# Optimization experiments

Hardware: AMD Instinct MI355X
Metric: run time of the kernel (lower is better)

Reference implementation:

```python
import jax, jax.numpy as jnp
import numpy as np

N_NODES = 50000
N_EDGES = 800000
N_GRAPHS = 512
IN_C, HID, OUT_C = 128, 256, 16


def _mlp(h, w1, b1, w2, b2):
    # PyG-style 2-layer MLP: Linear -> ReLU -> Linear (plain last layer)
    return jax.nn.relu(h @ w1 + b1) @ w2 + b2


def setup_inputs() -> dict:
    key = jax.random.key(0)
    ks = jax.random.split(key, 16)
    x = jax.random.normal(ks[0], (N_NODES, IN_C), dtype=jnp.float32)
    edge_index = jax.random.randint(ks[1], (2, N_EDGES), 0, N_NODES, dtype=jnp.int64)
    batch = jnp.sort(jax.random.randint(ks[2], (N_NODES,), 0, N_GRAPHS, dtype=jnp.int64))

    def lin(k, fan_in, fan_out):
        s = 1.0 / np.sqrt(fan_in)
        return jax.random.uniform(k, (fan_in, fan_out), jnp.float32, -s, s)

    inp = {"x": x, "edge_index": edge_index, "batch": batch}
    dims = [(IN_C, HID), (HID, HID), (HID, HID)]
    ki = 3
    for li, (din, dh) in enumerate(dims):
        inp[f"c{li}_w1"] = lin(ks[ki], din, dh); ki += 1
        inp[f"c{li}_b1"] = jnp.zeros((dh,), jnp.float32)
        inp[f"c{li}_w2"] = lin(ks[ki], dh, dh); ki += 1
        inp[f"c{li}_b2"] = jnp.zeros((dh,), jnp.float32)
    inp["out_w1"] = lin(ks[ki], HID, HID); ki += 1
    inp["out_b1"] = jnp.zeros((HID,), jnp.float32)
    inp["out_w2"] = lin(ks[ki], HID, OUT_C); ki += 1
    inp["out_b2"] = jnp.zeros((OUT_C,), jnp.float32)
    return inp


def reference(x, edge_index, batch,
              c0_w1, c0_b1, c0_w2, c0_b2,
              c1_w1, c1_b1, c1_w2, c1_b2,
              c2_w1, c2_b1, c2_w2, c2_b2,
              out_w1, out_b1, out_w2, out_b2):
    src, dst = edge_index[0], edge_index[1]
    params = [(c0_w1, c0_b1, c0_w2, c0_b2),
              (c1_w1, c1_b1, c1_w2, c1_b2),
              (c2_w1, c2_b1, c2_w2, c2_b2)]
    h = x
    for (w1, b1, w2, b2) in params:
        # GINConv with eps=0: MLP(x + sum_{j in N(i)} x_j)
        agg = jax.ops.segment_sum(h[src], dst, num_segments=N_NODES)
        h = _mlp(h + agg, w1, b1, w2, b2)
        h = jax.nn.relu(h)
        # dropout: identity (eval mode)
    # global mean pool over graphs
    sums = jax.ops.segment_sum(h, batch, num_segments=N_GRAPHS)
    counts = jax.ops.segment_sum(jnp.ones((N_NODES,), h.dtype), batch, num_segments=N_GRAPHS)
    pooled = sums / jnp.maximum(counts, 1.0)[:, None]
    return _mlp(pooled, out_w1, out_b1, out_w2, out_b2)
```

## Files before the change

kernel.cpp:

```cpp
#include <hip/hip_runtime.h>

#define N_NODES 50000
#define N_EDGES 800000
#define N_GRAPHS 512
#define IN_C 128
#define HID 256
#define OUT_C 16

typedef __attribute__((ext_vector_type(8))) short short8;
typedef __attribute__((ext_vector_type(4))) float f32x4;

__device__ __forceinline__ float bf2f(unsigned short u) {
    return __uint_as_float(((unsigned int)u) << 16);
}
__device__ __forceinline__ unsigned short f2bf(float f) {
    unsigned int u = __float_as_uint(f);
    u += 0x7fff + ((u >> 16) & 1);
    return (unsigned short)(u >> 16);
}

#define PLANE_ELEMS ((long)N_NODES * 32)

struct PrepArgs {
    const float* x;
    const float* w[6];
    ushort* xbf;
    ushort* wt[6];
    int* deg;
    float* sums;
};

__global__ __launch_bounds__(256) void prep_kernel(PrepArgs a) {
    const int X4    = N_NODES * IN_C / 4;
    const int TW    = IN_C * HID;
    const int TH    = HID * HID;
    const int TBASE = X4;
    const int TEND  = TBASE + TW + 5 * TH;
    const int D4    = N_NODES / 4;
    const int DBASE = TEND;
    const int SBASE = DBASE + D4;
    const int S4    = N_GRAPHS * HID / 4;
    const long total = (long)SBASE + S4;

    long stride = (long)gridDim.x * blockDim.x;
    for (long i = (long)blockIdx.x * blockDim.x + threadIdx.x; i < total; i += stride) {
        if (i < X4) {
            float4 v = ((const float4*)a.x)[i];
            ushort4 o;
            o.x = f2bf(v.x); o.y = f2bf(v.y); o.z = f2bf(v.z); o.w = f2bf(v.w);
            long e = i * 4;
            int node = (int)(e >> 7);
            int col  = (int)(e & 127);
            long off = (long)(col >> 5) * PLANE_ELEMS + (long)node * 32 + (col & 31);
            *(ushort4*)(a.xbf + off) = o;
        } else if (i < TEND) {
            long r = i - TBASE;
            int wi, shift;
            long off;
            if (r < TW) { wi = 0; shift = 7; off = r; }
            else { r -= TW; wi = 1 + (int)(r / TH); shift = 8; off = r % TH; }
            int n = (int)(off >> shift);
            int k = (int)(off - ((long)n << shift));
            a.wt[wi][off] = f2bf(a.w[wi][(long)k * HID + n]);
        } else if (i < SBASE) {
            ((int4*)a.deg)[i - DBASE] = make_int4(0, 0, 0, 0);
        } else {
            ((float4*)a.sums)[i - SBASE] = make_float4(0.f, 0.f, 0.f, 0.f);
        }
    }
}

__global__ void deg_kernel(const int* __restrict__ dst, int* __restrict__ deg) {
    int e = blockIdx.x * blockDim.x + threadIdx.x;
    if (e < N_EDGES) atomicAdd(&deg[dst[e]], 1);
}

__global__ __launch_bounds__(256) void scan_block(const int* __restrict__ deg,
                                                  int* __restrict__ partial,
                                                  int* __restrict__ blockSums) {
    __shared__ int s[256];
    int t = threadIdx.x;
    int i = blockIdx.x * 256 + t;
    int v = (i < N_NODES) ? deg[i] : 0;
    s[t] = v;
    __syncthreads();
    #pragma unroll
    for (int off = 1; off < 256; off <<= 1) {
        int add = (t >= off) ? s[t - off] : 0;
        __syncthreads();
        s[t] += add;
        __syncthreads();
    }
    if (i < N_NODES) partial[i] = s[t] - v;
    if (t == 255) blockSums[blockIdx.x] = s[255];
}

__global__ __launch_bounds__(256) void add_offsets_fused(
    const int* __restrict__ partial, const int* __restrict__ blockSums,
    int* __restrict__ rowptr, int* __restrict__ cursor, int nb) {
    __shared__ int s[256];
    __shared__ int myOff;
    int t = threadIdx.x;
    int v = (t < nb) ? blockSums[t] : 0;
    s[t] = v;
    __syncthreads();
    #pragma unroll
    for (int off = 1; off < 256; off <<= 1) {
        int add = (t >= off) ? s[t - off] : 0;
        __syncthreads();
        s[t] += add;
        __syncthreads();
    }
    if (t == blockIdx.x) myOff = s[t] - v;
    __syncthreads();
    int i = blockIdx.x * 256 + t;
    if (i < N_NODES) {
        int r = partial[i] + myOff;
        rowptr[i] = r;
        cursor[i] = r;
    }
    if (i == 0) rowptr[N_NODES] = N_EDGES;
}

__global__ void bucket_edges(const int* __restrict__ src, const int* __restrict__ dst,
                             int* __restrict__ cursor, int* __restrict__ srcSorted) {
    int e = blockIdx.x * blockDim.x + threadIdx.x;
    if (e >= N_EDGES) return;
    int p = atomicAdd(&cursor[dst[e]], 1);
    srcSorted[p] = src[e];
}

template <int C>
__global__ __launch_bounds__(256) void gin_aggregate_planar(
    const ushort* __restrict__ hp,
    const int* __restrict__ rowptr,
    const int* __restrict__ srcIdx,
    ushort* __restrict__ out)
{
    constexpr int NC  = C / 32;
    constexpr int PER = 8 / NC;

    int b  = blockIdx.x;
    int x8 = b & 7;
    int chunk   = x8 / PER;
    int nodeblk = (b >> 3) * PER + (x8 & (PER - 1));

    int lane = threadIdx.x & 63;
    int wave = threadIdx.x >> 6;
    int grp  = lane >> 2;
    int l    = lane & 3;
    int node = nodeblk * 64 + wave * 16 + grp;
    if (node >= N_NODES) return;

    const ushort* plane = hp + (long)chunk * PLANE_ELEMS + l * 8;

    float acc[8];
    {
        short8 sv = *(const short8*)(plane + (long)node * 32);
        #pragma unroll
        for (int v = 0; v < 8; ++v) acc[v] = bf2f((unsigned short)sv[v]);
    }

    int beg = rowptr[node], end = rowptr[node + 1];
    int k = beg;
    for (; k + 4 <= end; k += 4) {
        int si[4];
        #pragma unroll
        for (int u = 0; u < 4; ++u) si[u] = srcIdx[k + u];
        short8 r[4];
        #pragma unroll
        for (int u = 0; u < 4; ++u) r[u] = *(const short8*)(plane + (long)si[u] * 32);
        #pragma unroll
        for (int u = 0; u < 4; ++u)
            #pragma unroll
            for (int v = 0; v < 8; ++v) acc[v] += bf2f((unsigned short)r[u][v]);
    }
    for (; k < end; ++k) {
        short8 r = *(const short8*)(plane + (long)srcIdx[k] * 32);
        #pragma unroll
        for (int v = 0; v < 8; ++v) acc[v] += bf2f((unsigned short)r[v]);
    }

    short8 o;
    #pragma unroll
    for (int v = 0; v < 8; ++v) o[v] = (short)f2bf(acc[v]);
    *(short8*)(out + (long)node * C + chunk * 32 + l * 8) = o;
}

template <int K1, bool FUSE_POOL>
__global__ __launch_bounds__(256, 4) void gin_mlp(
    const ushort* __restrict__ A,
    const ushort* __restrict__ w1t,
    const float* __restrict__ b1,
    const ushort* __restrict__ w2t,
    const float* __restrict__ b2,
    ushort* __restrict__ out,
    const int* __restrict__ batch,
    float* __restrict__ sums,
    int M)
{
    __shared__ short Ls[2048 * 8];

    constexpr int NCH1 = K1 / 8;
    constexpr int NSLOT1 = 64 * NCH1;

    int t = threadIdx.x;
    int lane = t & 63;
    int wv = t >> 6;
    int quad = lane >> 4;
    int l15 = lane & 15;
    int swz = l15 & 7;
    int row0 = blockIdx.x * 64;
    int col0 = wv * 64;

    #pragma unroll
    for (int c = 0; c < NSLOT1; c += 256) {
        int s = c + t;
        int row = s / NCH1;
        int kcs = s & (NCH1 - 1);
        int kc = kcs ^ (row & 7);
        int grow = row0 + row;
        if (grow >= M) grow = M - 1;
        short8 v = *(const short8*)(A + (long)grow * K1 + kc * 8);
        *(short8*)&Ls[s * 8] = v;
    }
    __syncthreads();

    const f32x4 zero = {0.f, 0.f, 0.f, 0.f};
    f32x4 acc[4][4];

    #pragma unroll
    for (int i = 0; i < 4; ++i)
        #pragma unroll
        for (int j = 0; j < 4; ++j) acc[i][j] = zero;

    long brow[4];
    #pragma unroll
    for (int j = 0; j < 4; ++j)
        brow[j] = (long)(col0 + j * 16 + l15) * K1;

    #pragma unroll
    for (int s = 0; s < K1 / 32; ++s) {
        short8 a[4], b[4];
        #pragma unroll
        for (int i = 0; i < 4; ++i) {
            int row = i * 16 + l15;
            int slot = row * NCH1 + ((s * 4 + quad) ^ swz);
            a[i] = *(const short8*)&Ls[slot * 8];
        }
        #pragma unroll
        for (int j = 0; j < 4; ++j)
            b[j] = *(const short8*)(w1t + brow[j] + s * 32 + quad * 8);
        #pragma unroll
        for (int i = 0; i < 4; ++i)
            #pragma unroll
            for (int j = 0; j < 4; ++j)
                acc[i][j] = __builtin_amdgcn_mfma_f32_16x16x32_bf16(a[i], b[j], acc[i][j], 0, 0, 0);
    }
    __syncthreads();

    {
        float bv[4];
        #pragma unroll
        for (int j = 0; j < 4; ++j) bv[j] = b1[col0 + j * 16 + l15];
        #pragma unroll
        for (int i = 0; i < 4; ++i)
            #pragma unroll
            for (int j = 0; j < 4; ++j) {
                int col = col0 + j * 16 + l15;
                int kc2 = col >> 3, sub = col & 7;
                #pragma unroll
                for (int r = 0; r < 4; ++r) {
                    int row = i * 16 + quad * 4 + r;
                    int slot = row * 32 + (kc2 ^ (row & 7));
                    float o = fmaxf(acc[i][j][r] + bv[j], 0.f);
                    Ls[slot * 8 + sub] = (short)f2bf(o);
                }
            }
    }
    __syncthreads();

    #pragma unroll
    for (int i = 0; i < 4; ++i)
        #pragma unroll
        for (int j = 0; j < 4; ++j) acc[i][j] = zero;

    long brow2[4];
    #pragma unroll
    for (int j = 0; j < 4; ++j)
        brow2[j] = (long)(col0 + j * 16 + l15) * 256;

    #pragma unroll
    for (int s = 0; s < 8; ++s) {
        short8 a[4], b[4];
        #pragma unroll
        for (int i = 0; i < 4; ++i) {
            int row = i * 16 + l15;
            int slot = row * 32 + ((s * 4 + quad) ^ swz);
            a[i] = *(const short8*)&Ls[slot * 8];
        }
        #pragma unroll
        for (int j = 0; j < 4; ++j)
            b[j] = *(const short8*)(w2t + brow2[j] + s * 32 + quad * 8);
        #pragma unroll
        for (int i = 0; i < 4; ++i)
            #pragma unroll
            for (int j = 0; j < 4; ++j)
                acc[i][j] = __builtin_amdgcn_mfma_f32_16x16x32_bf16(a[i], b[j], acc[i][j], 0, 0, 0);
    }

    float bv[4];
    #pragma unroll
    for (int j = 0; j < 4; ++j) bv[j] = b2[col0 + j * 16 + l15];

    if constexpr (!FUSE_POOL) {
        #pragma unroll
        for (int i = 0; i < 4; ++i)
            #pragma unroll
            for (int r = 0; r < 4; ++r) {
                int row = row0 + i * 16 + quad * 4 + r;
                if (row >= M) continue;
                #pragma unroll
                for (int j = 0; j < 4; ++j) {
                    int col = col0 + j * 16 + l15;
                    float o = fmaxf(acc[i][j][r] + bv[j], 0.f);
                    out[(long)(col >> 5) * PLANE_ELEMS + (long)row * 32 + (col & 31)] = f2bf(o);
                }
            }
    } else {
        float pacc[4];
        #pragma unroll
        for (int j = 0; j < 4; ++j) pacc[j] = 0.f;
        int cur = -1;
        #pragma unroll
        for (int i = 0; i < 4; ++i) {
            #pragma unroll
            for (int r = 0; r < 4; ++r) {
                int row = row0 + i * 16 + quad * 4 + r;
                if (row >= M) continue;
                int g = batch[row];
                if (g != cur) {
                    if (cur >= 0) {
                        #pragma unroll
                        for (int j = 0; j < 4; ++j)
                            atomicAdd(&sums[(long)cur * 256 + col0 + j * 16 + l15], pacc[j]);
                    }
                    cur = g;
                    #pragma unroll
                    for (int j = 0; j < 4; ++j) pacc[j] = 0.f;
                }
                #pragma unroll
                for (int j = 0; j < 4; ++j)
                    pacc[j] += fmaxf(acc[i][j][r] + bv[j], 0.f);
            }
        }
        if (cur >= 0) {
            #pragma unroll
            for (int j = 0; j < 4; ++j)
                atomicAdd(&sums[(long)cur * 256 + col0 + j * 16 + l15], pacc[j]);
        }
    }
}

__global__ __launch_bounds__(256) void final_mlp_kernel(
    const float* __restrict__ sums, const int* __restrict__ batch,
    const float* __restrict__ w1, const float* __restrict__ b1,
    const float* __restrict__ w2, const float* __restrict__ b2,
    float* __restrict__ out) {
    __shared__ float row[HID];
    __shared__ float hid[HID];
    __shared__ int cntS;
    int g = blockIdx.x;
    int t = threadIdx.x;
    if (t == 0) {
        int lo = 0, hi = N_NODES;
        while (lo < hi) { int m = (lo + hi) >> 1; if (batch[m] < g) lo = m + 1; else hi = m; }
        int lo2 = lo, hi2 = N_NODES;
        while (lo2 < hi2) { int m = (lo2 + hi2) >> 1; if (batch[m] < g + 1) lo2 = m + 1; else hi2 = m; }
        cntS = lo2 - lo;
    }
    __syncthreads();
    float cnt = fmaxf((float)cntS, 1.0f);
    row[t] = sums[(long)g * HID + t] / cnt;
    __syncthreads();
    float acc = b1[t];
    for (int k = 0; k < HID; ++k) acc += row[k] * w1[k * HID + t];
    hid[t] = fmaxf(acc, 0.f);
    __syncthreads();
    if (t < OUT_C) {
        float o = b2[t];
        for (int k = 0; k < HID; ++k) o += hid[k] * w2[k * OUT_C + t];
        out[(long)g * OUT_C + t] = o;
    }
}

extern "C" void kernel_launch(void* const* d_in, const int* in_sizes, int n_in,
                              void* d_out, int out_size, void* d_ws, size_t ws_size,
                              hipStream_t stream) {
    const float* x     = (const float*)d_in[0];
    const int*   ei    = (const int*)d_in[1];
    const int*   batch = (const int*)d_in[2];
    const int*   src   = ei;
    const int*   dst   = ei + N_EDGES;

    const float* c_w1[3] = { (const float*)d_in[3],  (const float*)d_in[7],  (const float*)d_in[11] };
    const float* c_b1[3] = { (const float*)d_in[4],  (const float*)d_in[8],  (const float*)d_in[12] };
    const float* c_w2[3] = { (const float*)d_in[5],  (const float*)d_in[9],  (const float*)d_in[13] };
    const float* c_b2[3] = { (const float*)d_in[6],  (const float*)d_in[10], (const float*)d_in[14] };
    const float* out_w1 = (const float*)d_in[15];
    const float* out_b1 = (const float*)d_in[16];
    const float* out_w2 = (const float*)d_in[17];
    const float* out_b2 = (const float*)d_in[18];

    char* p = (char*)d_ws;
    auto alloc = [&](size_t bytes) {
        char* r = p;
        p += (bytes + 15) & ~(size_t)15;
        return r;
    };
    ushort* xbf  = (ushort*)alloc((size_t)N_NODES * IN_C * 2);
    ushort* bufA = (ushort*)alloc((size_t)N_NODES * HID * 2);
    ushort* bufB = (ushort*)alloc((size_t)N_NODES * HID * 2);
    ushort* wt[6];
    wt[0] = (ushort*)alloc((size_t)IN_C * HID * 2);
    for (int i = 1; i < 6; ++i) wt[i] = (ushort*)alloc((size_t)HID * HID * 2);
    float* sums   = (float*)alloc((size_t)N_GRAPHS * HID * 4);
    int* deg       = (int*)alloc((size_t)N_NODES * 4);
    int* rowptr    = (int*)alloc((size_t)(N_NODES + 1) * 4);
    int* blockSums = (int*)alloc(256 * 4);
    int* cursor    = (int*)alloc((size_t)N_NODES * 4);
    int* srcSorted = (int*)alloc((size_t)N_EDGES * 4);

    const int nb = (N_NODES + 255) / 256;

    {
        PrepArgs a;
        a.x = x;
        a.w[0] = c_w1[0]; a.w[1] = c_w2[0];
        a.w[2] = c_w1[1]; a.w[3] = c_w2[1];
        a.w[4] = c_w1[2]; a.w[5] = c_w2[2];
        a.xbf = xbf;
        for (int i = 0; i < 6; ++i) a.wt[i] = wt[i];
        a.deg = deg;
        a.sums = sums;
        prep_kernel<<<2048, 256, 0, stream>>>(a);
    }

    deg_kernel<<<(N_EDGES + 255) / 256, 256, 0, stream>>>(dst, deg);
    scan_block<<<nb, 256, 0, stream>>>(deg, rowptr, blockSums);
    add_offsets_fused<<<nb, 256, 0, stream>>>(rowptr, blockSums, rowptr, cursor, nb);
    bucket_edges<<<(N_EDGES + 255) / 256, 256, 0, stream>>>(src, dst, cursor, srcSorted);

    const int nodeBlks = (N_NODES + 63) / 64;
    const int aggX128  = nodeBlks * (IN_C / 32);
    const int aggX256  = nodeBlks * (HID / 32);
    const int mlpGrid  = (N_NODES + 63) / 64;

    gin_aggregate_planar<IN_C><<<aggX128, 256, 0, stream>>>(xbf, rowptr, srcSorted, bufB);
    gin_mlp<IN_C, false><<<mlpGrid, 256, 0, stream>>>(bufB, wt[0], c_b1[0], wt[1], c_b2[0],
                                                      bufA, batch, sums, N_NODES);

    gin_aggregate_planar<HID><<<aggX256, 256, 0, stream>>>(bufA, rowptr, srcSorted, bufB);
    gin_mlp<HID, false><<<mlpGrid, 256, 0, stream>>>(bufB, wt[2], c_b1[1], wt[3], c_b2[1],
                                                     bufA, batch, sums, N_NODES);

    gin_aggregate_planar<HID><<<aggX256, 256, 0, stream>>>(bufA, rowptr, srcSorted, bufB);
    gin_mlp<HID, true><<<mlpGrid, 256, 0, stream>>>(bufB, wt[4], c_b1[2], wt[5], c_b2[2],
                                                    bufA, batch, sums, N_NODES);

    final_mlp_kernel<<<N_GRAPHS, 256, 0, stream>>>(sums, batch, out_w1, out_b1,
                                                   out_w2, out_b2, (float*)d_out);
}
```

Measured before the change: 464.3 us.

## Use 8 waves per MLP block and hold weight fragments in registers

The fused GIN MLP kernel now launches 512 threads (8 waves), and each wave computes 32 output columns instead of 64. Each wave preloads all of its layer-1 weight fragments into registers before the A tile is staged. It then loads its layer-2 weights during the epilogue, instead of fetching B fragments inside the MFMA loop. This is meant to raise wave-level parallelism and hide global weight-load latency behind the LDS staging and MFMA work. The cost is more register pressure from the 16 short8 fragments, and each A fragment read from LDS now feeds only two MFMAs, which lowers arithmetic intensity per LDS read.

```diff
diff --git a/kernel.cpp b/kernel.cpp
--- a/kernel.cpp
+++ b/kernel.cpp
@@ -188,7 +188,7 @@
 }
 
 template <int K1, bool FUSE_POOL>
-__global__ __launch_bounds__(256, 4) void gin_mlp(
+__global__ __launch_bounds__(512, 4) void gin_mlp(
     const ushort* __restrict__ A,
     const ushort* __restrict__ w1t,
     const float* __restrict__ b1,
@@ -203,6 +203,7 @@
 
     constexpr int NCH1 = K1 / 8;
     constexpr int NSLOT1 = 64 * NCH1;
+    constexpr int NS1 = K1 / 32;
 
     int t = threadIdx.x;
     int lane = t & 63;
@@ -211,10 +212,21 @@
     int l15 = lane & 15;
     int swz = l15 & 7;
     int row0 = blockIdx.x * 64;
-    int col0 = wv * 64;
-
-    #pragma unroll
-    for (int c = 0; c < NSLOT1; c += 256) {
+    int col0 = wv * 32;
+
+    short8 bw[16];
+    #pragma unroll
+    for (int s = 0; s < NS1; ++s)
+        #pragma unroll
+        for (int j = 0; j < 2; ++j)
+            bw[s * 2 + j] = *(const short8*)(w1t + (long)(col0 + j * 16 + l15) * K1 + s * 32 + quad * 8);
+
+    float bv[2];
+    #pragma unroll
+    for (int j = 0; j < 2; ++j) bv[j] = b1[col0 + j * 16 + l15];
+
+    #pragma unroll
+    for (int c = 0; c < NSLOT1; c += 512) {
         int s = c + t;
         int row = s / NCH1;
         int kcs = s & (NCH1 - 1);
@@ -227,91 +239,68 @@
     __syncthreads();
 
     const f32x4 zero = {0.f, 0.f, 0.f, 0.f};
-    f32x4 acc[4][4];
-
+    f32x4 acc[4][2];
     #pragma unroll
     for (int i = 0; i < 4; ++i)
         #pragma unroll
-        for (int j = 0; j < 4; ++j) acc[i][j] = zero;
-
-    long brow[4];
-    #pragma unroll
-    for (int j = 0; j < 4; ++j)
-        brow[j] = (long)(col0 + j * 16 + l15) * K1;
-
-    #pragma unroll
-    for (int s = 0; s < K1 / 32; ++s) {
-        short8 a[4], b[4];
+        for (int j = 0; j < 2; ++j) acc[i][j] = zero;
+
+    #pragma unroll
+    for (int s = 0; s < NS1; ++s) {
         #pragma unroll
         for (int i = 0; i < 4; ++i) {
             int row = i * 16 + l15;
             int slot = row * NCH1 + ((s * 4 + quad) ^ swz);
-            a[i] = *(const short8*)&Ls[slot * 8];
-        }
-        #pragma unroll
-        for (int j = 0; j < 4; ++j)
-            b[j] = *(const short8*)(w1t + brow[j] + s * 32 + quad * 8);
-        #pragma unroll
-        for (int i = 0; i < 4; ++i)
+            short8 a = *(const short8*)&Ls[slot * 8];
+            acc[i][0] = __builtin_amdgcn_mfma_f32_16x16x32_bf16(a, bw[s * 2 + 0], acc[i][0], 0, 0, 0);
+            acc[i][1] = __builtin_amdgcn_mfma_f32_16x16x32_bf16(a, bw[s * 2 + 1], acc[i][1], 0, 0, 0);
+        }
+    }
+
+    #pragma unroll
+    for (int s = 0; s < 8; ++s)
+        #pragma unroll
+        for (int j = 0; j < 2; ++j)
+            bw[s * 2 + j] = *(const short8*)(w2t + (long)(col0 + j * 16 + l15) * 256 + s * 32 + quad * 8);
+
+    __syncthreads();
+
+    #pragma unroll
+    for (int i = 0; i < 4; ++i)
+        #pragma unroll
+        for (int j = 0; j < 2; ++j) {
+            int col = col0 + j * 16 + l15;
+            int kc2 = col >> 3, sub = col & 7;
             #pragma unroll
-            for (int j = 0; j < 4; ++j)
-                acc[i][j] = __builtin_amdgcn_mfma_f32_16x16x32_bf16(a[i], b[j], acc[i][j], 0, 0, 0);
-    }
-    __syncthreads();
-
-    {
-        float bv[4];
-        #pragma unroll
-        for (int j = 0; j < 4; ++j) bv[j] = b1[col0 + j * 16 + l15];
-        #pragma unroll
-        for (int i = 0; i < 4; ++i)
-            #pragma unroll
-            for (int j = 0; j < 4; ++j) {
-                int col = col0 + j * 16 + l15;
-                int kc2 = col >> 3, sub = col & 7;
-                #pragma unroll
-                for (int r = 0; r < 4; ++r) {
-                    int row = i * 16 + quad * 4 + r;
-                    int slot = row * 32 + (kc2 ^ (row & 7));
-                    float o = fmaxf(acc[i][j][r] + bv[j], 0.f);
-                    Ls[slot * 8 + sub] = (short)f2bf(o);
-                }
+            for (int r = 0; r < 4; ++r) {
+                int row = i * 16 + quad * 4 + r;
+                int slot = row * 32 + (kc2 ^ (row & 7));
+                float o = fmaxf(acc[i][j][r] + bv[j], 0.f);
+                Ls[slot * 8 + sub] = (short)f2bf(o);
             }
-    }
+        }
+
+    #pragma unroll
+    for (int j = 0; j < 2; ++j) bv[j] = b2[col0 + j * 16 + l15];
+
     __syncthreads();
 
     #pragma unroll
     for (int i = 0; i < 4; ++i)
         #pragma unroll
-        for (int j = 0; j < 4; ++j) acc[i][j] = zero;
-
-    long brow2[4];
-    #pragma unroll
-    for (int j = 0; j < 4; ++j)
-        brow2[j] = (long)(col0 + j * 16 + l15) * 256;
+        for (int j = 0; j < 2; ++j) acc[i][j] = zero;
 
     #pragma unroll
     for (int s = 0; s < 8; ++s) {
-        short8 a[4], b[4];
         #pragma unroll
         for (int i = 0; i < 4; ++i) {
             int row = i * 16 + l15;
             int slot = row * 32 + ((s * 4 + quad) ^ swz);
-            a[i] = *(const short8*)&Ls[slot * 8];
-        }
-        #pragma unroll
-        for (int j = 0; j < 4; ++j)
-            b[j] = *(const short8*)(w2t + brow2[j] + s * 32 + quad * 8);
-        #pragma unroll
-        for (int i = 0; i < 4; ++i)
-            #pragma unroll
-            for (int j = 0; j < 4; ++j)
-                acc[i][j] = __builtin_amdgcn_mfma_f32_16x16x32_bf16(a[i], b[j], acc[i][j], 0, 0, 0);
-    }
-
-    float bv[4];
-    #pragma unroll
-    for (int j = 0; j < 4; ++j) bv[j] = b2[col0 + j * 16 + l15];
+            short8 a = *(const short8*)&Ls[slot * 8];
+            acc[i][0] = __builtin_amdgcn_mfma_f32_16x16x32_bf16(a, bw[s * 2 + 0], acc[i][0], 0, 0, 0);
+            acc[i][1] = __builtin_amdgcn_mfma_f32_16x16x32_bf16(a, bw[s * 2 + 1], acc[i][1], 0, 0, 0);
+        }
+    }
 
     if constexpr (!FUSE_POOL) {
         #pragma unroll
@@ -321,16 +310,16 @@
                 int row = row0 + i * 16 + quad * 4 + r;
                 if (row >= M) continue;
                 #pragma unroll
-                for (int j = 0; j < 4; ++j) {
+                for (int j = 0; j < 2; ++j) {
                     int col = col0 + j * 16 + l15;
                     float o = fmaxf(acc[i][j][r] + bv[j], 0.f);
                     out[(long)(col >> 5) * PLANE_ELEMS + (long)row * 32 + (col & 31)] = f2bf(o);
                 }
             }
     } else {
-        float pacc[4];
-        #pragma unroll
-        for (int j = 0; j < 4; ++j) pacc[j] = 0.f;
+        float pacc[2];
+        #pragma unroll
+        for (int j = 0; j < 2; ++j) pacc[j] = 0.f;
         int cur = -1;
         #pragma unroll
         for (int i = 0; i < 4; ++i) {
@@ -342,21 +331,21 @@
                 if (g != cur) {
                     if (cur >= 0) {
                         #pragma unroll
-                        for (int j = 0; j < 4; ++j)
+                        for (int j = 0; j < 2; ++j)
                             atomicAdd(&sums[(long)cur * 256 + col0 + j * 16 + l15], pacc[j]);
                     }
                     cur = g;
                     #pragma unroll
-                    for (int j = 0; j < 4; ++j) pacc[j] = 0.f;
+                    for (int j = 0; j < 2; ++j) pacc[j] = 0.f;
                 }
                 #pragma unroll
-                for (int j = 0; j < 4; ++j)
+                for (int j = 0; j < 2; ++j)
                     pacc[j] += fmaxf(acc[i][j][r] + bv[j], 0.f);
             }
         }
         if (cur >= 0) {
             #pragma unroll
-            for (int j = 0; j < 4; ++j)
+            for (int j = 0; j < 2; ++j)
                 atomicAdd(&sums[(long)cur * 256 + col0 + j * 16 + l15], pacc[j]);
         }
     }
@@ -457,15 +446,15 @@
     const int mlpGrid  = (N_NODES + 63) / 64;
 
     gin_aggregate_planar<IN_C><<<aggX128, 256, 0, stream>>>(xbf, rowptr, srcSorted, bufB);
-    gin_mlp<IN_C, false><<<mlpGrid, 256, 0, stream>>>(bufB, wt[0], c_b1[0], wt[1], c_b2[0],
+    gin_mlp<IN_C, false><<<mlpGrid, 512, 0, stream>>>(bufB, wt[0], c_b1[0], wt[1], c_b2[0],
                                                       bufA, batch, sums, N_NODES);
 
     gin_aggregate_planar<HID><<<aggX256, 256, 0, stream>>>(bufA, rowptr, srcSorted, bufB);
-    gin_mlp<HID, false><<<mlpGrid, 256, 0, stream>>>(bufB, wt[2], c_b1[1], wt[3], c_b2[1],
+    gin_mlp<HID, false><<<mlpGrid, 512, 0, stream>>>(bufB, wt[2], c_b1[1], wt[3], c_b2[1],
                                                      bufA, batch, sums, N_NODES);
 
     gin_aggregate_planar<HID><<<aggX256, 256, 0, stream>>>(bufA, rowptr, srcSorted, bufB);
-    gin_mlp<HID, true><<<mlpGrid, 256, 0, stream>>>(bufB, wt[4], c_b1[2], wt[5], c_b2[2],
+    gin_mlp<HID, true><<<mlpGrid, 512, 0, stream>>>(bufB, wt[4], c_b1[2], wt[5], c_b2[2],
                                                     bufA, batch, sums, N_NODES);
 
     final_mlp_kernel<<<N_GRAPHS, 256, 0, stream>>>(sums, batch, out_w1, out_b1,
```

Result: faster. 452.8 us (-2.5%).
